# Performance work log

Measured on AMD Instinct MI355X. Metric: run time of the kernel, lower is better.

The kernel has to match this reference:

```python
import jax, jax.numpy as jnp
import numpy as np

DIM = 384
NUM_HEADS = 12
WS = 8            # window_size
SS = 4            # shift_size
HEAD_DIM = DIM // NUM_HEADS
SCALE = HEAD_DIM ** -0.5
N = WS * WS       # tokens per window
EPS = 1e-5
MLP_HIDDEN = 4 * DIM

# relative position index (static, matches torch buffer construction)
_coords = np.stack(np.meshgrid(np.arange(WS), np.arange(WS), indexing='ij')).reshape(2, -1)
_rel = (_coords[:, :, None] - _coords[:, None, :]).transpose(1, 2, 0)  # [N,N,2]
_rel[..., 0] += WS - 1
_rel[..., 1] += WS - 1
_rel[..., 0] *= 2 * WS - 1
RPI = jnp.asarray(_rel.sum(-1))  # [N,N] int


def layer_norm(x, g, b):
    m = x.mean(-1, keepdims=True)
    v = ((x - m) ** 2).mean(-1, keepdims=True)
    return (x - m) / jnp.sqrt(v + EPS) * g + b


def window_partition(x):
    B, Hh, Ww, C = x.shape
    x = x.reshape(B, Hh // WS, WS, Ww // WS, WS, C).transpose(0, 1, 3, 2, 4, 5)
    return x.reshape(-1, WS, WS, C)


def window_reverse(w, Hh, Ww):
    B = w.shape[0] // ((Hh // WS) * (Ww // WS))
    x = w.reshape(B, Hh // WS, Ww // WS, WS, WS, -1).transpose(0, 1, 3, 2, 4, 5)
    return x.reshape(B, Hh, Ww, -1)


def attention_mask(Hp, Wp):
    # region id along each axis: 0 = [0, Hp-WS), 1 = [Hp-WS, Hp-SS), 2 = [Hp-SS, Hp)
    h_id = np.zeros(Hp, np.int32); h_id[Hp - WS:Hp - SS] = 1; h_id[Hp - SS:] = 2
    w_id = np.zeros(Wp, np.int32); w_id[Wp - WS:Wp - SS] = 1; w_id[Wp - SS:] = 2
    cnt = h_id[:, None] * 3 + w_id[None, :]                      # [Hp, Wp]
    img = jnp.asarray(cnt, jnp.float32).reshape(1, Hp, Wp, 1)
    mw = window_partition(img).reshape(-1, N)                    # [nW, N]
    am = mw[:, None, :] - mw[:, :, None]                         # [nW, N, N]
    return jnp.where(am != 0, jnp.float32(-100.0), jnp.float32(0.0))


def setup_inputs() -> dict:
    key = jax.random.key(0)
    ks = jax.random.split(key, 8)
    B, H, W = 32, 64, 64
    std = 0.02
    return {
        'x': jax.random.normal(ks[0], (B, H * W, DIM), jnp.float32),
        'qkv_w': jax.random.normal(ks[1], (DIM, 3 * DIM), jnp.float32) * std,
        'qkv_b': jnp.zeros((3 * DIM,), jnp.float32),
        'proj_w': jax.random.normal(ks[2], (DIM, DIM), jnp.float32) * std,
        'proj_b': jnp.zeros((DIM,), jnp.float32),
        'rpb_table': jax.random.normal(ks[3], ((2 * WS - 1) * (2 * WS - 1), NUM_HEADS), jnp.float32) * std,
        'n1_g': jnp.ones((DIM,), jnp.float32), 'n1_b': jnp.zeros((DIM,), jnp.float32),
        'n2_g': jnp.ones((DIM,), jnp.float32), 'n2_b': jnp.zeros((DIM,), jnp.float32),
        'fc1_w': jax.random.normal(ks[4], (DIM, MLP_HIDDEN), jnp.float32) * std,
        'fc1_b': jnp.zeros((MLP_HIDDEN,), jnp.float32),
        'fc2_w': jax.random.normal(ks[5], (MLP_HIDDEN, DIM), jnp.float32) * std,
        'fc2_b': jnp.zeros((DIM,), jnp.float32),
        'H': 64, 'W': 64,
    }


def reference(x, qkv_w, qkv_b, proj_w, proj_b, rpb_table, n1_g, n1_b, n2_g, n2_b,
              fc1_w, fc1_b, fc2_w, fc2_b, H, W):
    B, L, C = x.shape
    shortcut = x
    h = layer_norm(x, n1_g, n1_b).reshape(B, H, W, C)
    pad_r = (WS - W % WS) % WS
    pad_b = (WS - H % WS) % WS
    if pad_r or pad_b:
        h = jnp.pad(h, ((0, 0), (0, pad_b), (0, pad_r), (0, 0)))
    Hp, Wp = H + pad_b, W + pad_r
    shifted = jnp.roll(h, shift=(-SS, -SS), axis=(1, 2))
    xw = window_partition(shifted).reshape(-1, N, C)             # [B_, N, C]
    B_ = xw.shape[0]

    qkv = (xw @ qkv_w + qkv_b).reshape(B_, N, 3, NUM_HEADS, HEAD_DIM)
    q = qkv[:, :, 0].transpose(0, 2, 1, 3) * SCALE               # [B_, h, N, d]
    k = qkv[:, :, 1].transpose(0, 2, 1, 3)
    v = qkv[:, :, 2].transpose(0, 2, 1, 3)

    attn = jnp.einsum('bhnd,bhmd->bhnm', q, k)                   # [B_, h, N, N]
    bias = rpb_table[RPI].transpose(2, 0, 1)                     # [h, N, N]
    attn = attn + bias[None]

    mask = attention_mask(Hp, Wp)                                # [nW, N, N]
    nW = mask.shape[0]
    attn = attn.reshape(B_ // nW, nW, NUM_HEADS, N, N) + mask[None, :, None]
    attn = jax.nn.softmax(attn.reshape(B_, NUM_HEADS, N, N), axis=-1)

    out = jnp.einsum('bhnm,bhmd->bhnd', attn, v)
    out = out.transpose(0, 2, 1, 3).reshape(B_, N, C)
    out = out @ proj_w + proj_b

    out = window_reverse(out.reshape(-1, WS, WS, C), Hp, Wp)
    out = jnp.roll(out, shift=(SS, SS), axis=(1, 2))
    out = out[:, :H, :W, :].reshape(B, H * W, C)

    x = shortcut + out
    h2 = layer_norm(x, n2_g, n2_b)
    mlp = jax.nn.gelu(h2 @ fc1_w + fc1_b, approximate=False) @ fc2_w + fc2_b
    return x + mlp
```

## Files before the change

kernel.cpp:

```cpp
#include <hip/hip_runtime.h>
#include <math.h>


#define ROWS_TOTAL 131072
#define NWIN_TOTAL 2048

typedef __attribute__((ext_vector_type(8))) __bf16 bf16x8;
typedef __attribute__((ext_vector_type(4))) float f32x4;
typedef __attribute__((ext_vector_type(8))) unsigned short ushort8;

__device__ __forceinline__ unsigned short f2bf(float f) {
  unsigned u = __builtin_bit_cast(unsigned, f);
  u = (u + 0x7fffu + ((u >> 16) & 1u)) >> 16;
  return (unsigned short)u;
}
__device__ __forceinline__ float bf2f(unsigned short u) {
  return __builtin_bit_cast(float, (unsigned)u << 16);
}

__device__ __forceinline__ void gload16(const void* g, void* l) {
  __builtin_amdgcn_global_load_lds(
      (const __attribute__((address_space(1))) unsigned int*)g,
      (__attribute__((address_space(3))) unsigned int*)l, 16, 0, 0);
}

__device__ __forceinline__ int gather_row(int win, int t) {
  int b = win >> 6, wi = (win >> 3) & 7, wj = win & 7;
  int gi = (wi * 8 + (t >> 3) + 4) & 63;
  int gj = (wj * 8 + (t & 7) + 4) & 63;
  return (b << 12) + (gi << 6) + gj;
}

__device__ __forceinline__ void frag_mma(const ushort* As_, const ushort* Bs_,
                                         int wr, int wc, int lane,
                                         f32x4 acc[4][4]) {
  const int go = (((lane >> 4) ^ ((lane >> 1) & 3)) << 3);
  const int lr = lane & 15;
  bf16x8 af[4], bfr[4];
#pragma unroll
  for (int mi = 0; mi < 4; ++mi)
    af[mi] = *(const bf16x8*)(As_ + (wr * 64 + mi * 16 + lr) * 32 + go);
#pragma unroll
  for (int nj = 0; nj < 4; ++nj)
    bfr[nj] = *(const bf16x8*)(Bs_ + (wc * 64 + nj * 16 + lr) * 32 + go);
#pragma unroll
  for (int mi = 0; mi < 4; ++mi)
#pragma unroll
    for (int nj = 0; nj < 4; ++nj)
      acc[mi][nj] = __builtin_amdgcn_mfma_f32_16x16x32_bf16(
          af[mi], bfr[nj], acc[mi][nj], 0, 0, 0);
}

#define VM8() asm volatile("s_waitcnt vmcnt(8)" ::: "memory")
#define VM4() asm volatile("s_waitcnt vmcnt(4)" ::: "memory")
#define VM0() asm volatile("s_waitcnt vmcnt(0)" ::: "memory")
#define SCB() __builtin_amdgcn_sched_barrier(0)
#define BARR() __builtin_amdgcn_s_barrier()

#define STG(B_, T_)                                   \
  { size_t ko = (size_t)(T_) * 64;                    \
    gload16(aS0 + ko, &As[B_][w * 1024]);             \
    gload16(aS1 + ko, &As[B_][w * 1024 + 512]);       \
    gload16(bS0 + ko, &Bs[B_][w * 1024]);             \
    gload16(bS1 + ko, &Bs[B_][w * 1024 + 512]); }

#define GEMM_PIPE(NK)                                               \
  {                                                                 \
    STG(0, 0);                                                      \
    STG(1, 1);                                                      \
    STG(2, 2);                                                      \
    VM8(); SCB(); BARR(); SCB();                                    \
    int cur = 0;                                                    \
    for (int t = 0; t < (NK); ++t) {                                \
      if (t + 3 < (NK)) STG((cur + 3) & 3, t + 3);                  \
      __builtin_amdgcn_s_setprio(1);                                \
      frag_mma(&As[cur][0], &Bs[cur][0], wr, wc, lane, acc);        \
      __builtin_amdgcn_s_setprio(0);                                \
      if (t + 3 < (NK)) { VM8(); }                                  \
      else if (t + 2 < (NK)) { VM4(); }                             \
      else { VM0(); }                                               \
      SCB(); BARR(); SCB();                                         \
      cur = (cur + 1) & 3;                                          \
    }                                                               \
  }

__global__ __launch_bounds__(256) void wprep_k(
    const float* __restrict__ qkvw, const float* __restrict__ projw,
    const float* __restrict__ fc1w, const float* __restrict__ fc2w,
    ushort* __restrict__ wq, ushort* __restrict__ wp,
    ushort* __restrict__ w1, ushort* __restrict__ w2) {
  int gid = blockIdx.x * 256 + threadIdx.x;
  const int S1 = 1152 * 384;
  const int S2 = S1 + 384 * 384;
  const int S3 = S2 + 1536 * 384;
  const int S4 = S3 + 384 * 1536;
  if (gid < S1) {
    int n = gid / 384, k = gid - n * 384;
    wq[gid] = f2bf(qkvw[(size_t)k * 1152 + n]);
  } else if (gid < S2) {
    int i = gid - S1, n = i / 384, k = i - n * 384;
    wp[i] = f2bf(projw[(size_t)k * 384 + n]);
  } else if (gid < S3) {
    int i = gid - S2, n = i / 384, k = i - n * 384;
    w1[i] = f2bf(fc1w[(size_t)k * 1536 + n]);
  } else if (gid < S4) {
    int i = gid - S3, n = i / 1536, k = i - n * 1536;
    w2[i] = f2bf(fc2w[(size_t)k * 384 + n]);
  }
}

__global__ __launch_bounds__(256) void ln_fused_k(
    const float* __restrict__ x, const float* __restrict__ g,
    const float* __restrict__ b, ushort* __restrict__ o) {
  int wid = threadIdx.x >> 6, lane = threadIdx.x & 63;
  int row = (blockIdx.x << 2) + wid;
  const float* p = x + (size_t)row * 384;
  float2 v[3];
  float s = 0.f, ss = 0.f;
#pragma unroll
  for (int c = 0; c < 3; ++c) {
    v[c] = *(const float2*)(p + lane * 2 + c * 128);
    s += v[c].x + v[c].y;
    ss += v[c].x * v[c].x + v[c].y * v[c].y;
  }
#pragma unroll
  for (int off = 1; off < 64; off <<= 1) {
    s += __shfl_xor(s, off);
    ss += __shfl_xor(ss, off);
  }
  float m = s * (1.f / 384.f);
  float r = rsqrtf(ss * (1.f / 384.f) - m * m + 1e-5f);
  ushort* op = o + (size_t)row * 384;
#pragma unroll
  for (int c = 0; c < 3; ++c) {
    float2 gg = *(const float2*)(g + lane * 2 + c * 128);
    float2 bb = *(const float2*)(b + lane * 2 + c * 128);
    union { ushort u[2]; unsigned w; } pk;
    pk.u[0] = f2bf((v[c].x - m) * r * gg.x + bb.x);
    pk.u[1] = f2bf((v[c].y - m) * r * gg.y + bb.y);
    *(unsigned*)(op + lane * 2 + c * 128) = pk.w;
  }
}

__global__ __launch_bounds__(256) void qkv_mfma_k(
    const ushort* __restrict__ xln, const ushort* __restrict__ wq,
    const float* __restrict__ qkvb, ushort* __restrict__ qd,
    ushort* __restrict__ kd, ushort* __restrict__ vd, int wc0) {
  __shared__ __align__(16) ushort As[4][4096];
  __shared__ __align__(16) ushort Bs[4][4096];
  __shared__ int rowS[128];
  const int tid = threadIdx.x;
  const int w = tid >> 6, lane = tid & 63;
  const int wr = w >> 1, wc = w & 1;
  int p, bm;
  {
    int lin = blockIdx.y * 9 + blockIdx.x;
    if ((gridDim.y & 7) == 0) {
      int xcd = lin & 7, q = lin >> 3;
      p = q % 9; bm = (q / 9) * 8 + xcd;
    } else { p = blockIdx.x; bm = blockIdx.y; }
  }
  const int n0 = p * 128;
  if (tid < 128) {
    int win = wc0 + bm * 2 + (tid >> 6);
    rowS[tid] = gather_row(win, tid & 63);
  }
  __syncthreads();
  const int rA = w * 32 + (lane >> 2);
  const int sle = (((lane & 3) ^ ((lane >> 3) & 3)) << 4);
  const char* aS0 = (const char*)xln + (size_t)rowS[rA] * 768 + sle;
  const char* aS1 = (const char*)xln + (size_t)rowS[rA + 16] * 768 + sle;
  const char* bS0 = (const char*)wq + (size_t)(n0 + rA) * 768 + sle;
  const char* bS1 = (const char*)wq + (size_t)(n0 + rA + 16) * 768 + sle;
  f32x4 acc[4][4];
#pragma unroll
  for (int i = 0; i < 4; ++i)
#pragma unroll
    for (int j = 0; j < 4; ++j) acc[i][j] = (f32x4)(0.f);
  GEMM_PIPE(12);
  const float scale = 0.17677669529663687f;
#pragma unroll
  for (int mi = 0; mi < 4; ++mi) {
#pragma unroll
    for (int r = 0; r < 4; ++r) {
      int rr = wr * 64 + mi * 16 + ((lane >> 4) << 2) + r;
      int w_rel = bm * 2 + (rr >> 6), t = rr & 63;
#pragma unroll
      for (int nj = 0; nj < 4; ++nj) {
        int nc = n0 + wc * 64 + nj * 16 + (lane & 15);
        float v = acc[mi][nj][r] + qkvb[nc];
        int qi = nc / 384, rem = nc - qi * 384;
        int hh = rem >> 5, d = rem & 31;
        ushort* base = (qi == 0) ? qd : (qi == 1 ? kd : vd);
        if (qi == 0) v *= scale;
        base[(((size_t)w_rel * 12 + hh) << 11) + (t << 5) + d] = f2bf(v);
      }
    }
  }
}

__global__ __launch_bounds__(128) void attn_k(
    const ushort* __restrict__ q, const ushort* __restrict__ k,
    const ushort* __restrict__ v, const float* __restrict__ rpb,
    ushort* __restrict__ ao, int wc0) {
  __shared__ __align__(16) float kbuf[2][64][32];
  __shared__ __align__(16) float vbuf[2][64][32];
  __shared__ float bias[2][232];
  __shared__ int region[64];
  const int tid = threadIdx.x;
  const int wid = tid >> 6, lane = tid & 63;
  const int w = blockIdx.x, win = wc0 + w;
  const int head = blockIdx.y * 2 + wid;
  if (tid < 64) {
    int wi = (win >> 3) & 7, wj = win & 7;
    int pi = wi * 8 + (tid >> 3), pj = wj * 8 + (tid & 7);
    int ri = pi < 56 ? 0 : (pi < 60 ? 1 : 2);
    int rj = pj < 56 ? 0 : (pj < 60 ? 1 : 2);
    region[tid] = ri * 3 + rj;
  }
  const size_t hb = ((size_t)w * 12 + head) * 2048;
  const ushort* kp = k + hb;
  const ushort* vp = v + hb;
#pragma unroll
  for (int s = 0; s < 4; ++s) {
    int f = s * 64 + lane;
    int r = f >> 2, c = (f & 3) * 8;
    ushort8 ku = *(const ushort8*)(kp + r * 32 + c);
    ushort8 vu = *(const ushort8*)(vp + r * 32 + c);
#pragma unroll
    for (int j = 0; j < 8; ++j) {
      kbuf[wid][r][c + j] = bf2f(ku[j]);
      vbuf[wid][r][c + j] = bf2f(vu[j]);
    }
  }
  for (int s = lane; s < 225; s += 64) bias[wid][s] = rpb[s * 12 + head];
  __syncthreads();
  const int i = lane;
  float qr[32];
  const ushort* qp = q + hb + (i << 5);
#pragma unroll
  for (int c = 0; c < 4; ++c) {
    ushort8 qu = *(const ushort8*)(qp + c * 8);
#pragma unroll
    for (int j = 0; j < 8; ++j) qr[c * 8 + j] = bf2f(qu[j]);
  }
  const int yi = i >> 3, xi = i & 7, regi = region[i];
  float sc[64];
  float mx = -3.0e38f;
#pragma unroll
  for (int j = 0; j < 64; ++j) {
    float a = 0.f;
#pragma unroll
    for (int c = 0; c < 32; c += 4) {
      float4 kv = *(float4*)&kbuf[wid][j][c];
      a = fmaf(qr[c], kv.x, a);
      a = fmaf(qr[c + 1], kv.y, a);
      a = fmaf(qr[c + 2], kv.z, a);
      a = fmaf(qr[c + 3], kv.w, a);
    }
    int dy = yi - (j >> 3) + 7, dx = xi - (j & 7) + 7;
    a += bias[wid][dy * 15 + dx];
    if (region[j] != regi) a -= 100.f;
    sc[j] = a;
    mx = fmaxf(mx, a);
  }
  float sum = 0.f;
#pragma unroll
  for (int j = 0; j < 64; ++j) {
    float e = __expf(sc[j] - mx);
    sc[j] = e;
    sum += e;
  }
  const float inv = 1.f / sum;
  float o[32];
#pragma unroll
  for (int c = 0; c < 32; ++c) o[c] = 0.f;
#pragma unroll
  for (int j = 0; j < 64; ++j) {
    float p = sc[j];
#pragma unroll
    for (int c = 0; c < 32; c += 4) {
      float4 vv = *(float4*)&vbuf[wid][j][c];
      o[c] = fmaf(p, vv.x, o[c]);
      o[c + 1] = fmaf(p, vv.y, o[c + 1]);
      o[c + 2] = fmaf(p, vv.z, o[c + 2]);
      o[c + 3] = fmaf(p, vv.w, o[c + 3]);
    }
  }
  ushort* op = ao + ((size_t)(w * 64 + i)) * 384 + (head << 5);
#pragma unroll
  for (int c = 0; c < 32; c += 8) {
    ushort8 pk;
#pragma unroll
    for (int j2 = 0; j2 < 8; ++j2) pk[j2] = f2bf(o[c + j2] * inv);
    *(ushort8*)(op + c) = pk;
  }
}

__global__ __launch_bounds__(256) void proj_mfma_k(
    const ushort* __restrict__ ao, const ushort* __restrict__ wp,
    const float* __restrict__ pb, const float* __restrict__ x,
    float* __restrict__ x2, int wc0) {
  __shared__ __align__(16) ushort As[4][4096];
  __shared__ __align__(16) ushort Bs[4][4096];
  const int tid = threadIdx.x;
  const int w = tid >> 6, lane = tid & 63;
  const int wr = w >> 1, wc = w & 1;
  int p, bm;
  {
    int lin = blockIdx.y * 3 + blockIdx.x;
    if ((gridDim.y & 7) == 0) {
      int xcd = lin & 7, q = lin >> 3;
      p = q % 3; bm = (q / 3) * 8 + xcd;
    } else { p = blockIdx.x; bm = blockIdx.y; }
  }
  const int n0 = p * 128;
  const int rA = w * 32 + (lane >> 2);
  const int sle = (((lane & 3) ^ ((lane >> 3) & 3)) << 4);
  const char* aS0 = (const char*)ao + (size_t)(bm * 128 + rA) * 768 + sle;
  const char* aS1 = aS0 + (size_t)16 * 768;
  const char* bS0 = (const char*)wp + (size_t)(n0 + rA) * 768 + sle;
  const char* bS1 = bS0 + (size_t)16 * 768;
  f32x4 acc[4][4];
#pragma unroll
  for (int i = 0; i < 4; ++i)
#pragma unroll
    for (int j = 0; j < 4; ++j) acc[i][j] = (f32x4)(0.f);
  GEMM_PIPE(12);
#pragma unroll
  for (int mi = 0; mi < 4; ++mi) {
#pragma unroll
    for (int r = 0; r < 4; ++r) {
      int rr = wr * 64 + mi * 16 + ((lane >> 4) << 2) + r;
      int gl = bm * 128 + rr;
      int gr = gather_row(wc0 + (gl >> 6), gl & 63);
#pragma unroll
      for (int nj = 0; nj < 4; ++nj) {
        int nc = n0 + wc * 64 + nj * 16 + (lane & 15);
        size_t idx = (size_t)gr * 384 + nc;
        x2[idx] = acc[mi][nj][r] + pb[nc] + x[idx];
      }
    }
  }
}

__global__ __launch_bounds__(256) void fc1_mfma_k(
    const ushort* __restrict__ x2ln, const ushort* __restrict__ w1,
    const float* __restrict__ fb, ushort* __restrict__ hm, int row0) {
  __shared__ __align__(16) ushort As[4][4096];
  __shared__ __align__(16) ushort Bs[4][4096];
  const int tid = threadIdx.x;
  const int w = tid >> 6, lane = tid & 63;
  const int wr = w >> 1, wc = w & 1;
  int p, bm;
  {
    int lin = blockIdx.y * 12 + blockIdx.x;
    if ((gridDim.y & 7) == 0) {
      int xcd = lin & 7, q = lin >> 3;
      p = q % 12; bm = (q / 12) * 8 + xcd;
    } else { p = blockIdx.x; bm = blockIdx.y; }
  }
  const int n0 = p * 128;
  const int rA = w * 32 + (lane >> 2);
  const int sle = (((lane & 3) ^ ((lane >> 3) & 3)) << 4);
  const char* aS0 = (const char*)x2ln + (size_t)(row0 + bm * 128 + rA) * 768 + sle;
  const char* aS1 = aS0 + (size_t)16 * 768;
  const char* bS0 = (const char*)w1 + (size_t)(n0 + rA) * 768 + sle;
  const char* bS1 = bS0 + (size_t)16 * 768;
  f32x4 acc[4][4];
#pragma unroll
  for (int i = 0; i < 4; ++i)
#pragma unroll
    for (int j = 0; j < 4; ++j) acc[i][j] = (f32x4)(0.f);
  GEMM_PIPE(12);
#pragma unroll
  for (int mi = 0; mi < 4; ++mi) {
#pragma unroll
    for (int r = 0; r < 4; ++r) {
      int rr = wr * 64 + mi * 16 + ((lane >> 4) << 2) + r;
      size_t lrow = (size_t)(bm * 128 + rr);
#pragma unroll
      for (int nj = 0; nj < 4; ++nj) {
        int nc = n0 + wc * 64 + nj * 16 + (lane & 15);
        float v = acc[mi][nj][r] + fb[nc];
        v = 0.5f * v * (1.f + erff(v * 0.70710678118654752f));
        hm[lrow * 1536 + nc] = f2bf(v);
      }
    }
  }
}

__global__ __launch_bounds__(256) void fc2_mfma_k(
    const ushort* __restrict__ hm, const ushort* __restrict__ w2,
    const float* __restrict__ fb, float* __restrict__ out, int row0) {
  __shared__ __align__(16) ushort As[4][4096];
  __shared__ __align__(16) ushort Bs[4][4096];
  const int tid = threadIdx.x;
  const int w = tid >> 6, lane = tid & 63;
  const int wr = w >> 1, wc = w & 1;
  int p, bm;
  {
    int lin = blockIdx.y * 3 + blockIdx.x;
    if ((gridDim.y & 7) == 0) {
      int xcd = lin & 7, q = lin >> 3;
      p = q % 3; bm = (q / 3) * 8 + xcd;
    } else { p = blockIdx.x; bm = blockIdx.y; }
  }
  const int n0 = p * 128;
  const int rA = w * 32 + (lane >> 2);
  const int sle = (((lane & 3) ^ ((lane >> 3) & 3)) << 4);
  const char* aS0 = (const char*)hm + (size_t)(bm * 128 + rA) * 3072 + sle;
  const char* aS1 = aS0 + (size_t)16 * 3072;
  const char* bS0 = (const char*)w2 + (size_t)(n0 + rA) * 3072 + sle;
  const char* bS1 = bS0 + (size_t)16 * 3072;
  f32x4 acc[4][4];
#pragma unroll
  for (int i = 0; i < 4; ++i)
#pragma unroll
    for (int j = 0; j < 4; ++j) acc[i][j] = (f32x4)(0.f);
  GEMM_PIPE(48);
#pragma unroll
  for (int mi = 0; mi < 4; ++mi) {
#pragma unroll
    for (int r = 0; r < 4; ++r) {
      int rr = wr * 64 + mi * 16 + ((lane >> 4) << 2) + r;
      size_t grow = (size_t)(row0 + bm * 128 + rr);
#pragma unroll
      for (int nj = 0; nj < 4; ++nj) {
        int nc = n0 + wc * 64 + nj * 16 + (lane & 15);
        size_t idx = grow * 384 + nc;
        out[idx] = out[idx] + acc[mi][nj][r] + fb[nc];
      }
    }
  }
}

extern "C" void kernel_launch(void* const* d_in, const int* in_sizes, int n_in,
                              void* d_out, int out_size, void* d_ws, size_t ws_size,
                              hipStream_t stream) {
  const float* x = (const float*)d_in[0];
  const float* qkv_w = (const float*)d_in[1];
  const float* qkv_b = (const float*)d_in[2];
  const float* proj_w = (const float*)d_in[3];
  const float* proj_b = (const float*)d_in[4];
  const float* rpb = (const float*)d_in[5];
  const float* n1g = (const float*)d_in[6];
  const float* n1b = (const float*)d_in[7];
  const float* n2g = (const float*)d_in[8];
  const float* n2b = (const float*)d_in[9];
  const float* fc1w = (const float*)d_in[10];
  const float* fc1b = (const float*)d_in[11];
  const float* fc2w = (const float*)d_in[12];
  const float* fc2b = (const float*)d_in[13];
  float* out = (float*)d_out;
  char* ws = (char*)d_ws;

  ushort* wq = (ushort*)ws;
  ushort* wp = wq + 442368;
  ushort* w1 = wp + 147456;
  ushort* w2 = w1 + 589824;
  ushort* xln = (ushort*)(ws + 3538944);
  char* scratch = ws + 3538944 + 100663296;
  size_t base = 3538944 + 100663296;
  size_t ssz = (ws_size > base) ? ws_size - base : 0;

  wprep_k<<<6912, 256, 0, stream>>>(qkv_w, proj_w, fc1w, fc2w, wq, wp, w1, w2);
  ln_fused_k<<<ROWS_TOTAL / 4, 256, 0, stream>>>(x, n1g, n1b, xln);

  const size_t perwin = 196608;
  int nwc = (int)(ssz / perwin);
  if (nwc > NWIN_TOTAL) nwc = NWIN_TOTAL;
  nwc &= ~15;
  if (nwc < 16) nwc = 16;
  ushort* qd = (ushort*)scratch;
  ushort* kd = qd + (size_t)nwc * 24576;
  ushort* vd = kd + (size_t)nwc * 24576;
  ushort* ao = vd + (size_t)nwc * 24576;
  for (int wc0 = 0; wc0 < NWIN_TOTAL; wc0 += nwc) {
    int nw = (NWIN_TOTAL - wc0 < nwc) ? (NWIN_TOTAL - wc0) : nwc;
    qkv_mfma_k<<<dim3(9, nw / 2), 256, 0, stream>>>(xln, wq, qkv_b, qd, kd, vd, wc0);
    attn_k<<<dim3(nw, 6), 128, 0, stream>>>(qd, kd, vd, rpb, ao, wc0);
    proj_mfma_k<<<dim3(3, nw / 2), 256, 0, stream>>>(ao, wp, proj_b, x, out, wc0);
  }

  ln_fused_k<<<ROWS_TOTAL / 4, 256, 0, stream>>>(out, n2g, n2b, xln);
  const size_t pergrp = 393216;
  int ngc = (int)(ssz / pergrp);
  if (ngc > 1024) ngc = 1024;
  ngc &= ~7;
  if (ngc < 8) ngc = 8;
  ushort* hm = (ushort*)scratch;
  for (int g0 = 0; g0 < 1024; g0 += ngc) {
    int ng = (1024 - g0 < ngc) ? (1024 - g0) : ngc;
    fc1_mfma_k<<<dim3(12, ng), 256, 0, stream>>>(xln, w1, fc1b, hm, g0 * 128);
    fc2_mfma_k<<<dim3(3, ng), 256, 0, stream>>>(hm, w2, fc2b, out, g0 * 128);
  }
}
```

Baseline: 1.446 ms.

## Use 256x128 tiles with BK=64 and 8-wave interleaved MFMA GEMM pipeline

Rewrites the shared GEMM core used by the qkv, proj, fc1 and fc2 kernels. Blocks now have 512 threads (8 waves) and compute 256x128 output tiles with a K-step of 64, using a 3-stage LDS ring and an XOR swizzle. Each K-step is split into four phases that interleave LDS fragment reads, global-to-LDS prefetch and MFMA quarters, separated by barriers and priority raises. The aim is more data reuse per tile, fewer loop iterations, and better overlap of memory traffic with matrix math. In exchange, each block needs about 144KB of LDS, which likely limits a CU to one block. The extra barriers per K-step also add synchronisation cost, and the host launch grids and chunk sizes are rescaled to match.

```diff
diff --git a/kernel.cpp b/kernel.cpp
--- a/kernel.cpp
+++ b/kernel.cpp
@@ -31,57 +31,85 @@
   return (b << 12) + (gi << 6) + gj;
 }
 
-__device__ __forceinline__ void frag_mma(const ushort* As_, const ushort* Bs_,
-                                         int wr, int wc, int lane,
-                                         f32x4 acc[4][4]) {
-  const int go = (((lane >> 4) ^ ((lane >> 1) & 3)) << 3);
-  const int lr = lane & 15;
-  bf16x8 af[4], bfr[4];
-#pragma unroll
-  for (int mi = 0; mi < 4; ++mi)
-    af[mi] = *(const bf16x8*)(As_ + (wr * 64 + mi * 16 + lr) * 32 + go);
-#pragma unroll
-  for (int nj = 0; nj < 4; ++nj)
-    bfr[nj] = *(const bf16x8*)(Bs_ + (wc * 64 + nj * 16 + lr) * 32 + go);
-#pragma unroll
-  for (int mi = 0; mi < 4; ++mi)
-#pragma unroll
-    for (int nj = 0; nj < 4; ++nj)
-      acc[mi][nj] = __builtin_amdgcn_mfma_f32_16x16x32_bf16(
-          af[mi], bfr[nj], acc[mi][nj], 0, 0, 0);
-}
-
-#define VM8() asm volatile("s_waitcnt vmcnt(8)" ::: "memory")
-#define VM4() asm volatile("s_waitcnt vmcnt(4)" ::: "memory")
+#define LGK0() asm volatile("s_waitcnt lgkmcnt(0)" ::: "memory")
+#define VM6() asm volatile("s_waitcnt vmcnt(6)" ::: "memory")
 #define VM0() asm volatile("s_waitcnt vmcnt(0)" ::: "memory")
 #define SCB() __builtin_amdgcn_sched_barrier(0)
 #define BARR() __builtin_amdgcn_s_barrier()
-
-#define STG(B_, T_)                                   \
-  { size_t ko = (size_t)(T_) * 64;                    \
-    gload16(aS0 + ko, &As[B_][w * 1024]);             \
-    gload16(aS1 + ko, &As[B_][w * 1024 + 512]);       \
-    gload16(bS0 + ko, &Bs[B_][w * 1024]);             \
-    gload16(bS1 + ko, &Bs[B_][w * 1024 + 512]); }
-
-#define GEMM_PIPE(NK)                                               \
-  {                                                                 \
-    STG(0, 0);                                                      \
-    STG(1, 1);                                                      \
-    STG(2, 2);                                                      \
-    VM8(); SCB(); BARR(); SCB();                                    \
-    int cur = 0;                                                    \
-    for (int t = 0; t < (NK); ++t) {                                \
-      if (t + 3 < (NK)) STG((cur + 3) & 3, t + 3);                  \
-      __builtin_amdgcn_s_setprio(1);                                \
-      frag_mma(&As[cur][0], &Bs[cur][0], wr, wc, lane, acc);        \
-      __builtin_amdgcn_s_setprio(0);                                \
-      if (t + 3 < (NK)) { VM8(); }                                  \
-      else if (t + 2 < (NK)) { VM4(); }                             \
-      else { VM0(); }                                               \
-      SCB(); BARR(); SCB();                                         \
-      cur = (cur + 1) & 3;                                          \
-    }                                                               \
+#define PRIO1() __builtin_amdgcn_s_setprio(1)
+#define PRIO0() __builtin_amdgcn_s_setprio(0)
+
+
+#define STGA(b_, c_, kt_)                                                   \
+  gload16(aSrcC[c_] + (size_t)(kt_) * 64,                                   \
+          (char*)&As[0][0] + (b_) * 32768 + (c_) * 8192 + w * 1024)
+#define STGB(b_, c_, kt_)                                                   \
+  gload16(bSrcC[c_] + (size_t)(kt_) * 64,                                   \
+          (char*)&Bs[0][0] + (b_) * 16384 + (c_) * 8192 + w * 1024)
+
+#define LDA(mi_)                                                            \
+  { a[mi_][0] = *(const bf16x8*)(AsB + aOff[mi_][0]);                       \
+    a[mi_][1] = *(const bf16x8*)(AsB + aOff[mi_][1]); }
+#define LDB(nj_)                                                            \
+  { b[nj_][0] = *(const bf16x8*)(BsB + bOff[nj_][0]);                       \
+    b[nj_][1] = *(const bf16x8*)(BsB + bOff[nj_][1]); }
+#define MM(mi_, nj_)                                                        \
+  { acc[mi_][nj_] = __builtin_amdgcn_mfma_f32_16x16x32_bf16(                \
+        a[mi_][0], b[nj_][0], acc[mi_][nj_], 0, 0, 0);                      \
+    acc[mi_][nj_] = __builtin_amdgcn_mfma_f32_16x16x32_bf16(                \
+        a[mi_][1], b[nj_][1], acc[mi_][nj_], 0, 0, 0); }
+
+#define GEMM_DECLS()                                                        \
+  f32x4 acc[4][4];                                                          \
+  bf16x8 a[4][2], b[4][2];                                                  \
+  int aOff[4][2], bOff[4][2];                                               \
+  _Pragma("unroll") for (int i_ = 0; i_ < 4; ++i_)                          \
+  _Pragma("unroll") for (int j_ = 0; j_ < 4; ++j_)                          \
+      acc[i_][j_] = (f32x4)(0.f);                                           \
+  _Pragma("unroll") for (int mi_ = 0; mi_ < 4; ++mi_)                       \
+  _Pragma("unroll") for (int ks_ = 0; ks_ < 2; ++ks_) {                     \
+    int sl_ = ((ks_ * 4 + hi) ^ (lr & 7)) * 8;                              \
+    aOff[mi_][ks_] = (wr * 64 + mi_ * 16 + lr) * 64 + sl_;                  \
+    bOff[mi_][ks_] = (wc * 64 + mi_ * 16 + lr) * 64 + sl_;                  \
+  }
+
+#define GEMM_CORE(NT)                                                       \
+  {                                                                         \
+    STGA(0, 0, 0); STGA(0, 1, 0); STGA(0, 2, 0); STGA(0, 3, 0);             \
+    STGB(0, 0, 0); STGB(0, 1, 0);                                           \
+    STGA(1, 0, 1); STGA(1, 1, 1); STGA(1, 2, 1); STGA(1, 3, 1);             \
+    STGB(1, 0, 1); STGB(1, 1, 1);                                           \
+    VM6(); SCB(); BARR(); SCB();                                            \
+    for (int t = 0; t < (NT); ++t) {                                        \
+      const int cur = t % 3, nxt = (t + 2) % 3;                             \
+      const bool st = (t + 2) < (NT);                                       \
+      const int kt = t + 2;                                                 \
+      const ushort* AsB = &As[0][0] + cur * 16384;                          \
+      const ushort* BsB = &Bs[0][0] + cur * 8192;                           \
+                                                                    \
+      LDA(0); LDA(1); LDB(0); LDB(1);                                       \
+      if (st) { STGA(nxt, 0, kt); STGA(nxt, 1, kt); }                       \
+      SCB(); BARR(); LGK0(); SCB();                                         \
+      PRIO1(); MM(0, 0); MM(0, 1); MM(1, 0); MM(1, 1); PRIO0();             \
+      SCB(); BARR(); SCB();                                                 \
+                                                                    \
+      LDB(2); LDB(3);                                                       \
+      if (st) { STGA(nxt, 2, kt); STGA(nxt, 3, kt); }                       \
+      SCB(); BARR(); LGK0(); SCB();                                         \
+      PRIO1(); MM(0, 2); MM(0, 3); MM(1, 2); MM(1, 3); PRIO0();             \
+      SCB(); BARR(); SCB();                                                 \
+                                                                    \
+      LDA(2); LDA(3);                                                       \
+      if (st) { STGB(nxt, 0, kt); }                                         \
+      SCB(); BARR(); LGK0(); SCB();                                         \
+      PRIO1(); MM(2, 2); MM(2, 3); MM(3, 2); MM(3, 3); PRIO0();             \
+      SCB(); BARR(); SCB();                                                 \
+                                                                    \
+      if (st) { STGB(nxt, 1, kt); }                                         \
+      PRIO1(); MM(2, 0); MM(2, 1); MM(3, 0); MM(3, 1); PRIO0();             \
+      if (st) { VM6(); } else { VM0(); }                                    \
+      SCB(); BARR(); SCB();                                                 \
+    }                                                                       \
   }
 
 __global__ __launch_bounds__(256) void wprep_k(
@@ -142,13 +170,13 @@
   }
 }
 
-__global__ __launch_bounds__(256) void qkv_mfma_k(
+__global__ __launch_bounds__(512, 2) void qkv_mfma_k(
     const ushort* __restrict__ xln, const ushort* __restrict__ wq,
     const float* __restrict__ qkvb, ushort* __restrict__ qd,
     ushort* __restrict__ kd, ushort* __restrict__ vd, int wc0) {
-  __shared__ __align__(16) ushort As[4][4096];
-  __shared__ __align__(16) ushort Bs[4][4096];
-  __shared__ int rowS[128];
+  __shared__ __align__(16) ushort As[3][16384];
+  __shared__ __align__(16) ushort Bs[3][8192];
+  __shared__ int rowS[256];
   const int tid = threadIdx.x;
   const int w = tid >> 6, lane = tid & 63;
   const int wr = w >> 1, wc = w & 1;
@@ -161,33 +189,30 @@
     } else { p = blockIdx.x; bm = blockIdx.y; }
   }
   const int n0 = p * 128;
-  if (tid < 128) {
-    int win = wc0 + bm * 2 + (tid >> 6);
-    rowS[tid] = gather_row(win, tid & 63);
-  }
+  if (tid < 256) rowS[tid] = gather_row(wc0 + bm * 4 + (tid >> 6), tid & 63);
   __syncthreads();
-  const int rA = w * 32 + (lane >> 2);
-  const int sle = (((lane & 3) ^ ((lane >> 3) & 3)) << 4);
-  const char* aS0 = (const char*)xln + (size_t)rowS[rA] * 768 + sle;
-  const char* aS1 = (const char*)xln + (size_t)rowS[rA + 16] * 768 + sle;
-  const char* bS0 = (const char*)wq + (size_t)(n0 + rA) * 768 + sle;
-  const char* bS1 = (const char*)wq + (size_t)(n0 + rA + 16) * 768 + sle;
-  f32x4 acc[4][4];
-#pragma unroll
-  for (int i = 0; i < 4; ++i)
-#pragma unroll
-    for (int j = 0; j < 4; ++j) acc[i][j] = (f32x4)(0.f);
-  GEMM_PIPE(12);
+  const int lr = lane & 15, hi = lane >> 4;
+  const int swz = ((tid & 7) ^ ((tid >> 3) & 7)) * 8;
+  const ushort* aSrcC[4];
+  const ushort* bSrcC[2];
+#pragma unroll
+  for (int c = 0; c < 4; ++c)
+    aSrcC[c] = xln + (size_t)rowS[c * 64 + (tid >> 3)] * 384 + swz;
+#pragma unroll
+  for (int c = 0; c < 2; ++c)
+    bSrcC[c] = wq + (size_t)(n0 + c * 64 + (tid >> 3)) * 384 + swz;
+  GEMM_DECLS();
+  GEMM_CORE(6);
   const float scale = 0.17677669529663687f;
 #pragma unroll
   for (int mi = 0; mi < 4; ++mi) {
 #pragma unroll
     for (int r = 0; r < 4; ++r) {
-      int rr = wr * 64 + mi * 16 + ((lane >> 4) << 2) + r;
-      int w_rel = bm * 2 + (rr >> 6), t = rr & 63;
+      int rr = wr * 64 + mi * 16 + (hi << 2) + r;
+      int w_rel = bm * 4 + (rr >> 6), t = rr & 63;
 #pragma unroll
       for (int nj = 0; nj < 4; ++nj) {
-        int nc = n0 + wc * 64 + nj * 16 + (lane & 15);
+        int nc = n0 + wc * 64 + nj * 16 + lr;
         float v = acc[mi][nj][r] + qkvb[nc];
         int qi = nc / 384, rem = nc - qi * 384;
         int hh = rem >> 5, d = rem & 31;
@@ -297,12 +322,12 @@
   }
 }
 
-__global__ __launch_bounds__(256) void proj_mfma_k(
+__global__ __launch_bounds__(512, 2) void proj_mfma_k(
     const ushort* __restrict__ ao, const ushort* __restrict__ wp,
     const float* __restrict__ pb, const float* __restrict__ x,
     float* __restrict__ x2, int wc0) {
-  __shared__ __align__(16) ushort As[4][4096];
-  __shared__ __align__(16) ushort Bs[4][4096];
+  __shared__ __align__(16) ushort As[3][16384];
+  __shared__ __align__(16) ushort Bs[3][8192];
   const int tid = threadIdx.x;
   const int w = tid >> 6, lane = tid & 63;
   const int wr = w >> 1, wc = w & 1;
@@ -315,28 +340,28 @@
     } else { p = blockIdx.x; bm = blockIdx.y; }
   }
   const int n0 = p * 128;
-  const int rA = w * 32 + (lane >> 2);
-  const int sle = (((lane & 3) ^ ((lane >> 3) & 3)) << 4);
-  const char* aS0 = (const char*)ao + (size_t)(bm * 128 + rA) * 768 + sle;
-  const char* aS1 = aS0 + (size_t)16 * 768;
-  const char* bS0 = (const char*)wp + (size_t)(n0 + rA) * 768 + sle;
-  const char* bS1 = bS0 + (size_t)16 * 768;
-  f32x4 acc[4][4];
-#pragma unroll
-  for (int i = 0; i < 4; ++i)
-#pragma unroll
-    for (int j = 0; j < 4; ++j) acc[i][j] = (f32x4)(0.f);
-  GEMM_PIPE(12);
+  const int lr = lane & 15, hi = lane >> 4;
+  const int swz = ((tid & 7) ^ ((tid >> 3) & 7)) * 8;
+  const ushort* aSrcC[4];
+  const ushort* bSrcC[2];
+#pragma unroll
+  for (int c = 0; c < 4; ++c)
+    aSrcC[c] = ao + (size_t)(bm * 256 + c * 64 + (tid >> 3)) * 384 + swz;
+#pragma unroll
+  for (int c = 0; c < 2; ++c)
+    bSrcC[c] = wp + (size_t)(n0 + c * 64 + (tid >> 3)) * 384 + swz;
+  GEMM_DECLS();
+  GEMM_CORE(6);
 #pragma unroll
   for (int mi = 0; mi < 4; ++mi) {
 #pragma unroll
     for (int r = 0; r < 4; ++r) {
-      int rr = wr * 64 + mi * 16 + ((lane >> 4) << 2) + r;
-      int gl = bm * 128 + rr;
+      int rr = wr * 64 + mi * 16 + (hi << 2) + r;
+      int gl = bm * 256 + rr;
       int gr = gather_row(wc0 + (gl >> 6), gl & 63);
 #pragma unroll
       for (int nj = 0; nj < 4; ++nj) {
-        int nc = n0 + wc * 64 + nj * 16 + (lane & 15);
+        int nc = n0 + wc * 64 + nj * 16 + lr;
         size_t idx = (size_t)gr * 384 + nc;
         x2[idx] = acc[mi][nj][r] + pb[nc] + x[idx];
       }
@@ -344,11 +369,11 @@
   }
 }
 
-__global__ __launch_bounds__(256) void fc1_mfma_k(
+__global__ __launch_bounds__(512, 2) void fc1_mfma_k(
     const ushort* __restrict__ x2ln, const ushort* __restrict__ w1,
     const float* __restrict__ fb, ushort* __restrict__ hm, int row0) {
-  __shared__ __align__(16) ushort As[4][4096];
-  __shared__ __align__(16) ushort Bs[4][4096];
+  __shared__ __align__(16) ushort As[3][16384];
+  __shared__ __align__(16) ushort Bs[3][8192];
   const int tid = threadIdx.x;
   const int w = tid >> 6, lane = tid & 63;
   const int wr = w >> 1, wc = w & 1;
@@ -361,27 +386,28 @@
     } else { p = blockIdx.x; bm = blockIdx.y; }
   }
   const int n0 = p * 128;
-  const int rA = w * 32 + (lane >> 2);
-  const int sle = (((lane & 3) ^ ((lane >> 3) & 3)) << 4);
-  const char* aS0 = (const char*)x2ln + (size_t)(row0 + bm * 128 + rA) * 768 + sle;
-  const char* aS1 = aS0 + (size_t)16 * 768;
-  const char* bS0 = (const char*)w1 + (size_t)(n0 + rA) * 768 + sle;
-  const char* bS1 = bS0 + (size_t)16 * 768;
-  f32x4 acc[4][4];
-#pragma unroll
-  for (int i = 0; i < 4; ++i)
-#pragma unroll
-    for (int j = 0; j < 4; ++j) acc[i][j] = (f32x4)(0.f);
-  GEMM_PIPE(12);
+  const int lr = lane & 15, hi = lane >> 4;
+  const int swz = ((tid & 7) ^ ((tid >> 3) & 7)) * 8;
+  const ushort* aSrcC[4];
+  const ushort* bSrcC[2];
+#pragma unroll
+  for (int c = 0; c < 4; ++c)
+    aSrcC[c] =
+        x2ln + (size_t)(row0 + bm * 256 + c * 64 + (tid >> 3)) * 384 + swz;
+#pragma unroll
+  for (int c = 0; c < 2; ++c)
+    bSrcC[c] = w1 + (size_t)(n0 + c * 64 + (tid >> 3)) * 384 + swz;
+  GEMM_DECLS();
+  GEMM_CORE(6);
 #pragma unroll
   for (int mi = 0; mi < 4; ++mi) {
 #pragma unroll
     for (int r = 0; r < 4; ++r) {
-      int rr = wr * 64 + mi * 16 + ((lane >> 4) << 2) + r;
-      size_t lrow = (size_t)(bm * 128 + rr);
+      int rr = wr * 64 + mi * 16 + (hi << 2) + r;
+      size_t lrow = (size_t)(bm * 256 + rr);
 #pragma unroll
       for (int nj = 0; nj < 4; ++nj) {
-        int nc = n0 + wc * 64 + nj * 16 + (lane & 15);
+        int nc = n0 + wc * 64 + nj * 16 + lr;
         float v = acc[mi][nj][r] + fb[nc];
         v = 0.5f * v * (1.f + erff(v * 0.70710678118654752f));
         hm[lrow * 1536 + nc] = f2bf(v);
@@ -390,11 +416,11 @@
   }
 }
 
-__global__ __launch_bounds__(256) void fc2_mfma_k(
+__global__ __launch_bounds__(512, 2) void fc2_mfma_k(
     const ushort* __restrict__ hm, const ushort* __restrict__ w2,
     const float* __restrict__ fb, float* __restrict__ out, int row0) {
-  __shared__ __align__(16) ushort As[4][4096];
-  __shared__ __align__(16) ushort Bs[4][4096];
+  __shared__ __align__(16) ushort As[3][16384];
+  __shared__ __align__(16) ushort Bs[3][8192];
   const int tid = threadIdx.x;
   const int w = tid >> 6, lane = tid & 63;
   const int wr = w >> 1, wc = w & 1;
@@ -407,27 +433,27 @@
     } else { p = blockIdx.x; bm = blockIdx.y; }
   }
   const int n0 = p * 128;
-  const int rA = w * 32 + (lane >> 2);
-  const int sle = (((lane & 3) ^ ((lane >> 3) & 3)) << 4);
-  const char* aS0 = (const char*)hm + (size_t)(bm * 128 + rA) * 3072 + sle;
-  const char* aS1 = aS0 + (size_t)16 * 3072;
-  const char* bS0 = (const char*)w2 + (size_t)(n0 + rA) * 3072 + sle;
-  const char* bS1 = bS0 + (size_t)16 * 3072;
-  f32x4 acc[4][4];
-#pragma unroll
-  for (int i = 0; i < 4; ++i)
-#pragma unroll
-    for (int j = 0; j < 4; ++j) acc[i][j] = (f32x4)(0.f);
-  GEMM_PIPE(48);
+  const int lr = lane & 15, hi = lane >> 4;
+  const int swz = ((tid & 7) ^ ((tid >> 3) & 7)) * 8;
+  const ushort* aSrcC[4];
+  const ushort* bSrcC[2];
+#pragma unroll
+  for (int c = 0; c < 4; ++c)
+    aSrcC[c] = hm + (size_t)(bm * 256 + c * 64 + (tid >> 3)) * 1536 + swz;
+#pragma unroll
+  for (int c = 0; c < 2; ++c)
+    bSrcC[c] = w2 + (size_t)(n0 + c * 64 + (tid >> 3)) * 1536 + swz;
+  GEMM_DECLS();
+  GEMM_CORE(24);
 #pragma unroll
   for (int mi = 0; mi < 4; ++mi) {
 #pragma unroll
     for (int r = 0; r < 4; ++r) {
-      int rr = wr * 64 + mi * 16 + ((lane >> 4) << 2) + r;
-      size_t grow = (size_t)(row0 + bm * 128 + rr);
+      int rr = wr * 64 + mi * 16 + (hi << 2) + r;
+      size_t grow = (size_t)(row0 + bm * 256 + rr);
 #pragma unroll
       for (int nj = 0; nj < 4; ++nj) {
-        int nc = n0 + wc * 64 + nj * 16 + (lane & 15);
+        int nc = n0 + wc * 64 + nj * 16 + lr;
         size_t idx = grow * 384 + nc;
         out[idx] = out[idx] + acc[mi][nj][r] + fb[nc];
       }
@@ -470,29 +496,29 @@
   const size_t perwin = 196608;
   int nwc = (int)(ssz / perwin);
   if (nwc > NWIN_TOTAL) nwc = NWIN_TOTAL;
-  nwc &= ~15;
-  if (nwc < 16) nwc = 16;
+  nwc &= ~3;
+  if (nwc < 4) nwc = 4;
   ushort* qd = (ushort*)scratch;
   ushort* kd = qd + (size_t)nwc * 24576;
   ushort* vd = kd + (size_t)nwc * 24576;
   ushort* ao = vd + (size_t)nwc * 24576;
   for (int wc0 = 0; wc0 < NWIN_TOTAL; wc0 += nwc) {
     int nw = (NWIN_TOTAL - wc0 < nwc) ? (NWIN_TOTAL - wc0) : nwc;
-    qkv_mfma_k<<<dim3(9, nw / 2), 256, 0, stream>>>(xln, wq, qkv_b, qd, kd, vd, wc0);
+    qkv_mfma_k<<<dim3(9, nw / 4), 512, 0, stream>>>(xln, wq, qkv_b, qd, kd, vd, wc0);
     attn_k<<<dim3(nw, 6), 128, 0, stream>>>(qd, kd, vd, rpb, ao, wc0);
-    proj_mfma_k<<<dim3(3, nw / 2), 256, 0, stream>>>(ao, wp, proj_b, x, out, wc0);
+    proj_mfma_k<<<dim3(3, nw / 4), 512, 0, stream>>>(ao, wp, proj_b, x, out, wc0);
   }
 
   ln_fused_k<<<ROWS_TOTAL / 4, 256, 0, stream>>>(out, n2g, n2b, xln);
-  const size_t pergrp = 393216;
+  const size_t pergrp = 786432;
   int ngc = (int)(ssz / pergrp);
-  if (ngc > 1024) ngc = 1024;
+  if (ngc > 512) ngc = 512;
   ngc &= ~7;
   if (ngc < 8) ngc = 8;
   ushort* hm = (ushort*)scratch;
-  for (int g0 = 0; g0 < 1024; g0 += ngc) {
-    int ng = (1024 - g0 < ngc) ? (1024 - g0) : ngc;
-    fc1_mfma_k<<<dim3(12, ng), 256, 0, stream>>>(xln, w1, fc1b, hm, g0 * 128);
-    fc2_mfma_k<<<dim3(3, ng), 256, 0, stream>>>(hm, w2, fc2b, out, g0 * 128);
-  }
-}
+  for (int g0 = 0; g0 < 512; g0 += ngc) {
+    int ng = (512 - g0 < ngc) ? (512 - g0) : ngc;
+    fc1_mfma_k<<<dim3(12, ng), 512, 0, stream>>>(xln, w1, fc1b, hm, g0 * 256);
+    fc2_mfma_k<<<dim3(3, ng), 512, 0, stream>>>(hm, w2, fc2b, out, g0 * 256);
+  }
+}
```

New measurement: 1.414 ms. 2.2% less time.
